# Kernel tuning notes

Hardware: AMD Instinct MI355X
Metric: run time of the kernel (lower is better)

The kernel has to match this reference:

```python
import jax, jax.numpy as jnp
import numpy as np

B, IN, OUT = 131072, 256, 256
BITWIDTH = 7.0


def setup_inputs() -> dict:
    key = jax.random.key(0)
    k1, k2 = jax.random.split(key)
    # simulated int8 activations (integer-valued float32)
    act_in = jax.random.randint(k1, (B, IN), -127, 128).astype(jnp.float32)
    # UniformWeights: xavier_uniform then weight_quant to the int8 grid
    limit = float(np.sqrt(6.0 / (IN + OUT)))
    w = jax.random.uniform(k2, (OUT, IN), minval=-limit, maxval=limit, dtype=jnp.float32)
    w_range = jnp.max(jnp.abs(w))
    weight_exp = (jnp.ceil(jnp.log2(w_range)) - 7.0).astype(jnp.int32)
    weight = jnp.round(w / w_range * 127.0)  # int8-valued float32 [OUT, IN]
    return {"act_in": act_in, "exp_in": jnp.int32(0), "weight": weight, "weight_exp": weight_exp}


def _round_shift(x, shift):
    # RoundShift: floor-div by 2**shift, add floor(|remainder| / 2**(shift-1)), clip to int8
    two_s = jnp.exp2(shift)
    rt = jnp.floor(x / two_s)
    prob = jnp.abs(x - rt * two_s)
    dec = jnp.floor(prob / jnp.exp2(shift - 1.0))
    return jnp.clip(rt + dec, -127.0, 127.0)


def reference(act_in, exp_in, weight, weight_exp):
    # int8 GEMM simulated in fp32 (exact: |acc| < 2^24)
    temp = act_in @ weight.T  # [B, OUT] int32 accumulator values
    # RangeEstimate: full-tensor abs-max -> bitwidth
    r = jnp.max(jnp.abs(temp))
    bw = jnp.where(r > 0, jnp.ceil(jnp.log2(jnp.maximum(r, 1.0))), 0.0)
    shift = bw - BITWIDTH
    pos = shift > 0
    safe_shift = jnp.maximum(shift, 1.0)
    rounded = _round_shift(temp, safe_shift)
    act_out = jnp.where(pos, rounded, temp).astype(jnp.int8)
    exp_sum = jnp.asarray(exp_in, jnp.int32) + jnp.asarray(weight_exp, jnp.int32)
    exp_out = (exp_sum + jnp.where(pos, shift, 0.0).astype(jnp.int32)).astype(jnp.int16)
    return act_out, exp_out
```

## Files before the change

kernel.cpp:

```cpp
#include <hip/hip_runtime.h>
#include <stdint.h>


#define M_ROWS 131072
#define NK 256
#define BM 64
#define BK 64
#define BKP 72

typedef __attribute__((ext_vector_type(8))) short bf16x8;
typedef __attribute__((ext_vector_type(4))) float f32x4;
typedef __attribute__((ext_vector_type(4))) unsigned int u32x4;

__device__ __forceinline__ uint32_t pack_bf16(float a, float b) {
  return (__float_as_uint(a) >> 16) | (__float_as_uint(b) & 0xFFFF0000u);
}

__device__ __forceinline__ void pack8(const float4 f0, const float4 f1, uint32_t pk[4]) {
  pk[0] = pack_bf16(f0.x, f0.y);
  pk[1] = pack_bf16(f0.z, f0.w);
  pk[2] = pack_bf16(f1.x, f1.y);
  pk[3] = pack_bf16(f1.z, f1.w);
}

__global__ __launch_bounds__(256, 3) void gemm_pass1(
    const float* __restrict__ act,
    const float* __restrict__ wgt,
    int* __restrict__ temp,
    int* __restrict__ gmax)
{
  __shared__ __align__(16) short As[BM * BKP];
  __shared__ __align__(16) short Bs[NK * BKP];
  __shared__ int smax;

  const int tid = threadIdx.x;
  if (tid == 0) smax = 0;

  const int bm   = blockIdx.x * BM;
  const int lane = tid & 63;
  const int wave = tid >> 6;
  const int lm   = lane & 15;
  const int lk   = lane >> 4;
  const int wn   = wave * 64;

  f32x4 acc[4][4] = {};

  for (int kt = 0; kt < NK; kt += BK) {
    uint32_t apk[2][4];
    uint32_t bpk[8][4];
#pragma unroll
    for (int j = 0; j < 2; ++j) {
      const int c = tid + (j << 8);
      const float* p = act + (size_t)(bm + (c >> 3)) * NK + kt + (c & 7) * 8;
      const float4 f0 = ((const float4*)p)[0];
      const float4 f1 = ((const float4*)p)[1];
      pack8(f0, f1, apk[j]);
    }
#pragma unroll
    for (int j = 0; j < 8; ++j) {
      const int c = tid + (j << 8);
      const float* p = wgt + (size_t)(c >> 3) * NK + kt + (c & 7) * 8;
      const float4 f0 = ((const float4*)p)[0];
      const float4 f1 = ((const float4*)p)[1];
      pack8(f0, f1, bpk[j]);
    }

    __syncthreads();
#pragma unroll
    for (int j = 0; j < 2; ++j) {
      const int c = tid + (j << 8);
      *(u32x4*)&As[(c >> 3) * BKP + (c & 7) * 8] = *(const u32x4*)apk[j];
    }
#pragma unroll
    for (int j = 0; j < 8; ++j) {
      const int c = tid + (j << 8);
      *(u32x4*)&Bs[(c >> 3) * BKP + (c & 7) * 8] = *(const u32x4*)bpk[j];
    }
    __syncthreads();

#pragma unroll
    for (int kk = 0; kk < BK; kk += 32) {
      bf16x8 af[4], bfr[4];
#pragma unroll
      for (int mi = 0; mi < 4; ++mi)
        af[mi] = *(const bf16x8*)&As[(mi * 16 + lm) * BKP + kk + lk * 8];
#pragma unroll
      for (int ni = 0; ni < 4; ++ni)
        bfr[ni] = *(const bf16x8*)&Bs[(wn + ni * 16 + lm) * BKP + kk + lk * 8];
#pragma unroll
      for (int mi = 0; mi < 4; ++mi)
#pragma unroll
        for (int ni = 0; ni < 4; ++ni)
          acc[mi][ni] = __builtin_amdgcn_mfma_f32_16x16x32_bf16(
              af[mi], bfr[ni], acc[mi][ni], 0, 0, 0);
    }
  }

  int imax = 0;
#pragma unroll
  for (int mi = 0; mi < 4; ++mi)
#pragma unroll
    for (int ni = 0; ni < 4; ++ni)
#pragma unroll
      for (int r = 0; r < 4; ++r) {
        const float v = acc[mi][ni][r];
        const int iv = (int)v;
        const int m = bm + mi * 16 + lk * 4 + r;
        const int n = wn + ni * 16 + lm;
        temp[(size_t)m * NK + n] = iv;
        const int a = iv < 0 ? -iv : iv;
        imax = a > imax ? a : imax;
      }
  atomicMax(&smax, imax);
  __syncthreads();
  if (tid == 0) atomicMax(gmax, smax);
}

__global__ void quant_pass2(int* __restrict__ temp,
                            const int* __restrict__ gmax,
                            const int* __restrict__ exp_in,
                            const int* __restrict__ wexp)
{
  const int r = *gmax;
  const int bw = (r <= 1) ? 0 : (32 - __clz(r - 1));
  const int shift = bw - 7;
  const bool pos = shift > 0;
  const int s = shift < 1 ? 1 : shift;

  const int total4 = (M_ROWS * NK) / 4;
  int4* p = (int4*)temp;
  const int idx = blockIdx.x * blockDim.x + threadIdx.x;
  const int stride = gridDim.x * blockDim.x;

  for (int i = idx; i < total4; i += stride) {
    const int4 t = p[i];
    int4 o;
#pragma unroll
    for (int j = 0; j < 4; ++j) {
      const int ti = ((const int*)&t)[j];
      int q;
      if (pos) {
        const int rt = ti >> s;
        const int dec = (ti - (rt << s)) >> (s - 1);
        q = rt + dec;
        q = q > 127 ? 127 : (q < -127 ? -127 : q);
      } else {
        q = (int)(signed char)(ti & 0xFF);
      }
      ((int*)&o)[j] = q;
    }
    p[i] = o;
  }

  if (idx == 0) {
    const int e = exp_in[0] + wexp[0] + (pos ? shift : 0);
    temp[(size_t)M_ROWS * NK] = (int)(short)e;
  }
}

extern "C" void kernel_launch(void* const* d_in, const int* in_sizes, int n_in,
                              void* d_out, int out_size, void* d_ws, size_t ws_size,
                              hipStream_t stream) {
  const float* act   = (const float*)d_in[0];
  const int* exp_in  = (const int*)d_in[1];
  const float* wgt   = (const float*)d_in[2];
  const int* wexp    = (const int*)d_in[3];
  int* gmax = (int*)d_ws;

  hipMemsetAsync(d_ws, 0, sizeof(int), stream);
  gemm_pass1<<<dim3(M_ROWS / BM), dim3(256), 0, stream>>>(act, wgt, (int*)d_out, gmax);
  quant_pass2<<<dim3(4096), dim3(256), 0, stream>>>((int*)d_out, gmax, exp_in, wexp);
}
```

Measured before the change: 289.1 us.

## Pre-convert weights to bf16, register-prefetch next K tile, use nontemporal traffic

Adds a small kernel that converts the fp32 weights to bf16 once per call, so each GEMM block loads half the weight bytes and skips the repeated packing. The GEMM loop now prefetches the next K tile into registers while the current tile runs on the MFMA units, overlapping global loads with compute. Output stores and the quantization pass use nontemporal loads and stores, and the per-block max is first reduced with wave shuffles, so there is one LDS atomic per wave instead of one per thread. The cost is an extra kernel launch and higher register pressure from the prefetch buffers.

```diff
diff --git a/kernel.cpp b/kernel.cpp
--- a/kernel.cpp
+++ b/kernel.cpp
@@ -10,22 +10,29 @@
 
 typedef __attribute__((ext_vector_type(8))) short bf16x8;
 typedef __attribute__((ext_vector_type(4))) float f32x4;
+typedef __attribute__((ext_vector_type(4))) float fv4;
+typedef __attribute__((ext_vector_type(4))) int iv4;
 typedef __attribute__((ext_vector_type(4))) unsigned int u32x4;
+typedef __attribute__((ext_vector_type(4))) unsigned short us4;
 
 __device__ __forceinline__ uint32_t pack_bf16(float a, float b) {
   return (__float_as_uint(a) >> 16) | (__float_as_uint(b) & 0xFFFF0000u);
 }
 
-__device__ __forceinline__ void pack8(const float4 f0, const float4 f1, uint32_t pk[4]) {
-  pk[0] = pack_bf16(f0.x, f0.y);
-  pk[1] = pack_bf16(f0.z, f0.w);
-  pk[2] = pack_bf16(f1.x, f1.y);
-  pk[3] = pack_bf16(f1.z, f1.w);
+__global__ void wconv(const float* __restrict__ w, unsigned short* __restrict__ wb) {
+  const int i = blockIdx.x * 256 + threadIdx.x;
+  const fv4 f = ((const fv4*)w)[i];
+  us4 o;
+  o.x = (unsigned short)(__float_as_uint(f.x) >> 16);
+  o.y = (unsigned short)(__float_as_uint(f.y) >> 16);
+  o.z = (unsigned short)(__float_as_uint(f.z) >> 16);
+  o.w = (unsigned short)(__float_as_uint(f.w) >> 16);
+  ((us4*)wb)[i] = o;
 }
 
 __global__ __launch_bounds__(256, 3) void gemm_pass1(
     const float* __restrict__ act,
-    const float* __restrict__ wgt,
+    const unsigned short* __restrict__ wgtb,
     int* __restrict__ temp,
     int* __restrict__ gmax)
 {
@@ -43,40 +50,50 @@
   const int lk   = lane >> 4;
   const int wn   = wave * 64;
 
+  const int arow = tid >> 3, aks = (tid & 7) * 8;
+  const int brow = tid >> 3, bks = (tid & 7) * 8;
+
+  uint32_t apk[2][4];
+  u32x4 breg[8];
+
+#pragma unroll
+  for (int j = 0; j < 2; ++j) {
+    const float* p = act + (size_t)(bm + arow + j * 32) * NK + aks;
+    const fv4 f0 = __builtin_nontemporal_load((const fv4*)p);
+    const fv4 f1 = __builtin_nontemporal_load((const fv4*)p + 1);
+    apk[j][0] = pack_bf16(f0.x, f0.y); apk[j][1] = pack_bf16(f0.z, f0.w);
+    apk[j][2] = pack_bf16(f1.x, f1.y); apk[j][3] = pack_bf16(f1.z, f1.w);
+  }
+#pragma unroll
+  for (int j = 0; j < 8; ++j)
+    breg[j] = *(const u32x4*)(wgtb + (size_t)(brow + j * 32) * NK + bks);
+
   f32x4 acc[4][4] = {};
 
   for (int kt = 0; kt < NK; kt += BK) {
-    uint32_t apk[2][4];
-    uint32_t bpk[8][4];
-#pragma unroll
-    for (int j = 0; j < 2; ++j) {
-      const int c = tid + (j << 8);
-      const float* p = act + (size_t)(bm + (c >> 3)) * NK + kt + (c & 7) * 8;
-      const float4 f0 = ((const float4*)p)[0];
-      const float4 f1 = ((const float4*)p)[1];
-      pack8(f0, f1, apk[j]);
-    }
-#pragma unroll
-    for (int j = 0; j < 8; ++j) {
-      const int c = tid + (j << 8);
-      const float* p = wgt + (size_t)(c >> 3) * NK + kt + (c & 7) * 8;
-      const float4 f0 = ((const float4*)p)[0];
-      const float4 f1 = ((const float4*)p)[1];
-      pack8(f0, f1, bpk[j]);
-    }
-
     __syncthreads();
 #pragma unroll
-    for (int j = 0; j < 2; ++j) {
-      const int c = tid + (j << 8);
-      *(u32x4*)&As[(c >> 3) * BKP + (c & 7) * 8] = *(const u32x4*)apk[j];
+    for (int j = 0; j < 2; ++j)
+      *(u32x4*)&As[(arow + j * 32) * BKP + aks] = *(const u32x4*)apk[j];
+#pragma unroll
+    for (int j = 0; j < 8; ++j)
+      *(u32x4*)&Bs[(brow + j * 32) * BKP + bks] = breg[j];
+    __syncthreads();
+
+    if (kt + BK < NK) {
+      const int ktn = kt + BK;
+#pragma unroll
+      for (int j = 0; j < 2; ++j) {
+        const float* p = act + (size_t)(bm + arow + j * 32) * NK + ktn + aks;
+        const fv4 f0 = __builtin_nontemporal_load((const fv4*)p);
+        const fv4 f1 = __builtin_nontemporal_load((const fv4*)p + 1);
+        apk[j][0] = pack_bf16(f0.x, f0.y); apk[j][1] = pack_bf16(f0.z, f0.w);
+        apk[j][2] = pack_bf16(f1.x, f1.y); apk[j][3] = pack_bf16(f1.z, f1.w);
+      }
+#pragma unroll
+      for (int j = 0; j < 8; ++j)
+        breg[j] = *(const u32x4*)(wgtb + (size_t)(brow + j * 32) * NK + ktn + bks);
     }
-#pragma unroll
-    for (int j = 0; j < 8; ++j) {
-      const int c = tid + (j << 8);
-      *(u32x4*)&Bs[(c >> 3) * BKP + (c & 7) * 8] = *(const u32x4*)bpk[j];
-    }
-    __syncthreads();
 
 #pragma unroll
     for (int kk = 0; kk < BK; kk += 32) {
@@ -107,11 +124,16 @@
         const int iv = (int)v;
         const int m = bm + mi * 16 + lk * 4 + r;
         const int n = wn + ni * 16 + lm;
-        temp[(size_t)m * NK + n] = iv;
+        __builtin_nontemporal_store(iv, &temp[(size_t)m * NK + n]);
         const int a = iv < 0 ? -iv : iv;
         imax = a > imax ? a : imax;
       }
-  atomicMax(&smax, imax);
+#pragma unroll
+  for (int off = 32; off; off >>= 1) {
+    const int o = __shfl_xor(imax, off, 64);
+    imax = o > imax ? o : imax;
+  }
+  if (lane == 0) atomicMax(&smax, imax);
   __syncthreads();
   if (tid == 0) atomicMax(gmax, smax);
 }
@@ -128,16 +150,16 @@
   const int s = shift < 1 ? 1 : shift;
 
   const int total4 = (M_ROWS * NK) / 4;
-  int4* p = (int4*)temp;
+  iv4* p = (iv4*)temp;
   const int idx = blockIdx.x * blockDim.x + threadIdx.x;
   const int stride = gridDim.x * blockDim.x;
 
   for (int i = idx; i < total4; i += stride) {
-    const int4 t = p[i];
-    int4 o;
+    const iv4 t = __builtin_nontemporal_load(&p[i]);
+    iv4 o;
 #pragma unroll
     for (int j = 0; j < 4; ++j) {
-      const int ti = ((const int*)&t)[j];
+      const int ti = t[j];
       int q;
       if (pos) {
         const int rt = ti >> s;
@@ -147,9 +169,9 @@
       } else {
         q = (int)(signed char)(ti & 0xFF);
       }
-      ((int*)&o)[j] = q;
+      o[j] = q;
     }
-    p[i] = o;
+    __builtin_nontemporal_store(o, &p[i]);
   }
 
   if (idx == 0) {
@@ -165,9 +187,11 @@
   const int* exp_in  = (const int*)d_in[1];
   const float* wgt   = (const float*)d_in[2];
   const int* wexp    = (const int*)d_in[3];
-  int* gmax = (int*)d_ws;
+  int* gmax          = (int*)d_ws;
+  unsigned short* wb = (unsigned short*)((char*)d_ws + 128);
 
-  hipMemsetAsync(d_ws, 0, sizeof(int), stream);
-  gemm_pass1<<<dim3(M_ROWS / BM), dim3(256), 0, stream>>>(act, wgt, (int*)d_out, gmax);
+  (void)hipMemsetAsync(d_ws, 0, sizeof(int), stream);
+  wconv<<<dim3(64), dim3(256), 0, stream>>>(wgt, wb);
+  gemm_pass1<<<dim3(M_ROWS / BM), dim3(256), 0, stream>>>(act, wb, (int*)d_out, gmax);
   quant_pass2<<<dim3(4096), dim3(256), 0, stream>>>((int*)d_out, gmax, exp_in, wexp);
 }
```

After: 303.2 us. +4.9%, slower.
